# Performance work log

Measured on AMD Instinct MI355X. Metric: run time of the kernel, lower is better.

## Reference

```python
import jax, jax.numpy as jnp
import numpy as np

N = 4096       # rows (batch * points)
D = 512        # d_model
H = 8          # num_heads


def setup_inputs() -> dict:
    key = jax.random.key(0)
    ks = jax.random.split(key, 11)
    s = 1.0 / np.sqrt(D).astype(np.float32)
    return {
        "x_q": jax.random.normal(ks[0], (N, D), jnp.float32),
        "x_k": jax.random.normal(ks[1], (N, D), jnp.float32),
        "x_v": jax.random.normal(ks[2], (N, D), jnp.float32),
        "Wq": jax.random.normal(ks[3], (D, D), jnp.float32) * s,
        "bq": jax.random.normal(ks[4], (D,), jnp.float32) * s,
        "Wk": jax.random.normal(ks[5], (D, D), jnp.float32) * s,
        "bk": jax.random.normal(ks[6], (D,), jnp.float32) * s,
        "Wv": jax.random.normal(ks[7], (D, D), jnp.float32) * s,
        "bv": jax.random.normal(ks[8], (D,), jnp.float32) * s,
        "Wo": jax.random.normal(ks[9], (D, D), jnp.float32) * s,
        "bo": jax.random.normal(ks[10], (D,), jnp.float32) * s,
    }


def reference(x_q, x_k, x_v, Wq, bq, Wk, bk, Wv, bv, Wo, bo):
    n, d = x_q.shape
    d_k = d // H
    # linear projections
    q = (x_q @ Wq + bq).reshape(n, H, d_k)  # chunk(dim=-1) == head split
    k = (x_k @ Wk + bk).reshape(n, H, d_k)
    v = (x_v @ Wv + bv).reshape(n, H, d_k)
    # channel-wise outer-product attention: scores[n,h,i,j] = q_i * k_j / sqrt(d_k)
    scale = jnp.asarray(1.0 / np.sqrt(d_k), q.dtype)
    scores = q[..., :, None] * k[..., None, :] * scale  # (n, H, d_k, d_k)
    p = jax.nn.softmax(scores, axis=-1)
    # attn output: p @ v over channel axis -> (n, H, d_k)
    x = jnp.einsum('nhij,nhj->nhi', p, v).reshape(n, d)  # head merge (cat dim=-1)
    return (x_q - x) @ Wo + bo
```

## Files before the change

kernel.cpp:

```cpp
#include <hip/hip_runtime.h>
#include <hip/hip_bf16.h>

#define NROWS 4096
#define DMODEL 512
#define NHEAD 8
#define DKH 64
#define ND (NROWS * DMODEL)
#define DD (DMODEL * DMODEL)

typedef unsigned short u16;
typedef __attribute__((ext_vector_type(8))) short short8;
typedef __attribute__((ext_vector_type(4))) float floatx4;

__device__ __forceinline__ u16 f2b(float f) {
    unsigned u = __float_as_uint(f);
    unsigned r = (u + 0x7fffu + ((u >> 16) & 1u)) >> 16;
    return (u16)r;
}
__device__ __forceinline__ float b2f(u16 v) {
    return __uint_as_float(((unsigned)v) << 16);
}
__device__ __forceinline__ void async16(const void* g, void* l) {
    __builtin_amdgcn_global_load_lds(g, l, 16, 0, 0);
}

__global__ __launch_bounds__(256) void convert_x(
    const float* __restrict__ s0, const float* __restrict__ s1,
    const float* __restrict__ s2, u16* __restrict__ d0, u16* __restrict__ d1,
    u16* __restrict__ d2, int nElem) {
    const float* s = blockIdx.z == 0 ? s0 : (blockIdx.z == 1 ? s1 : s2);
    u16* d = blockIdx.z == 0 ? d0 : (blockIdx.z == 1 ? d1 : d2);
    int i = (blockIdx.x * blockDim.x + threadIdx.x) * 4;
    if (i < nElem) {
        float4 v = *(const float4*)(s + i);
        ushort4 o;
        o.x = f2b(v.x); o.y = f2b(v.y); o.z = f2b(v.z); o.w = f2b(v.w);
        *(ushort4*)(d + i) = o;
    }
}

__global__ __launch_bounds__(256) void convert_w(
    const float* __restrict__ W0, const float* __restrict__ W1,
    const float* __restrict__ W2, const float* __restrict__ W3,
    u16* __restrict__ T0, u16* __restrict__ T1, u16* __restrict__ T2,
    u16* __restrict__ T3) {
    __shared__ float tile[32][33];
    int z = blockIdx.z;
    const float* W = z == 0 ? W0 : (z == 1 ? W1 : (z == 2 ? W2 : W3));
    u16* T = z == 0 ? T0 : (z == 1 ? T1 : (z == 2 ? T2 : T3));
    int n0 = blockIdx.x * 32, k0 = blockIdx.y * 32;
    int tx = threadIdx.x, ty = threadIdx.y;
#pragma unroll
    for (int r = 0; r < 32; r += 8)
        tile[ty + r][tx] = W[(size_t)(k0 + ty + r) * DMODEL + n0 + tx];
    __syncthreads();
#pragma unroll
    for (int r = 0; r < 32; r += 8) {
        int n = n0 + ty + r, k = k0 + tx;
        T[(size_t)n * DMODEL + k] = f2b(tile[tx][ty + r]);
    }
}

template <int OUTF>
__device__ __forceinline__ void gemm_bt_body(const u16* __restrict__ A,
                                             const u16* __restrict__ Bt,
                                             const float* __restrict__ bias,
                                             void* __restrict__ Cout) {
    __shared__ __align__(16) u16 lA[128 * 32];
    __shared__ __align__(16) u16 lB[64 * 32];
    const int tid = threadIdx.x;
    const int wave = tid >> 6, lane = tid & 63;
    const int tileM = blockIdx.y * 128;
    const int tileN = blockIdx.x * 64;
    const int wm = wave >> 1, wn = wave & 1;

    floatx4 acc[4][2];
#pragma unroll
    for (int i = 0; i < 4; i++)
#pragma unroll
        for (int j = 0; j < 2; j++) acc[i][j] = (floatx4){0.f, 0.f, 0.f, 0.f};

    const int lr4 = lane >> 2;
    const int ls = lane & 3;
    const int lrow = lane & 15;
    const int sk = lane >> 4;

    for (int t = 0; t < 16; ++t) {
        const int k0 = t * 32;
#pragma unroll
        for (int i = 0; i < 2; i++) {
            int c = wave * 2 + i;
            int r = c * 16 + lr4;
            int s = ls ^ ((r >> 1) & 3);
            async16(A + (size_t)(tileM + r) * 512 + k0 + s * 8, &lA[c * 512]);
        }
        {
            int r = wave * 16 + lr4;
            int s = ls ^ ((r >> 1) & 3);
            async16(Bt + (size_t)(tileN + r) * 512 + k0 + s * 8, &lB[wave * 512]);
        }
        __syncthreads();

        short8 bfr[2];
#pragma unroll
        for (int ni = 0; ni < 2; ++ni) {
            int r = wn * 32 + ni * 16 + lrow;
            int s = sk ^ ((r >> 1) & 3);
            bfr[ni] = *(const short8*)&lB[r * 32 + s * 8];
        }
#pragma unroll
        for (int mi = 0; mi < 4; ++mi) {
            int r = wm * 64 + mi * 16 + lrow;
            int s = sk ^ ((r >> 1) & 3);
            short8 af = *(const short8*)&lA[r * 32 + s * 8];
#pragma unroll
            for (int ni = 0; ni < 2; ++ni)
                acc[mi][ni] = __builtin_amdgcn_mfma_f32_16x16x32_bf16(
                    af, bfr[ni], acc[mi][ni], 0, 0, 0);
        }
        __syncthreads();
    }

#pragma unroll
    for (int mi = 0; mi < 4; ++mi) {
#pragma unroll
        for (int ni = 0; ni < 2; ++ni) {
            int col = tileN + wn * 32 + ni * 16 + lrow;
            float bv = bias[col];
#pragma unroll
            for (int r2 = 0; r2 < 4; r2++) {
                int row = tileM + wm * 64 + mi * 16 + sk * 4 + r2;
                float val = acc[mi][ni][r2] + bv;
                if (OUTF)
                    ((float*)Cout)[(size_t)row * 512 + col] = val;
                else
                    ((u16*)Cout)[(size_t)row * 512 + col] = f2b(val);
            }
        }
    }
}

__global__ __launch_bounds__(256) void proj3(
    const u16* __restrict__ xq, const u16* __restrict__ xk,
    const u16* __restrict__ xv, const u16* __restrict__ wtq,
    const u16* __restrict__ wtk, const u16* __restrict__ wtv,
    const float* __restrict__ bq, const float* __restrict__ bk,
    const float* __restrict__ bv, u16* __restrict__ Q, u16* __restrict__ K,
    u16* __restrict__ V) {
    int z = blockIdx.z;
    const u16* A = z == 0 ? xq : (z == 1 ? xk : xv);
    const u16* Bt = z == 0 ? wtq : (z == 1 ? wtk : wtv);
    const float* bias = z == 0 ? bq : (z == 1 ? bk : bv);
    u16* C = z == 0 ? Q : (z == 1 ? K : V);
    gemm_bt_body<0>(A, Bt, bias, C);
}

__global__ __launch_bounds__(256) void out_gemm(const u16* __restrict__ T,
                                                const u16* __restrict__ wto,
                                                const float* __restrict__ bo,
                                                float* __restrict__ C) {
    gemm_bt_body<1>(T, wto, bo, C);
}

__global__ __launch_bounds__(256) void attn_kernel(
    const u16* __restrict__ Qb, const u16* __restrict__ Kb,
    const u16* __restrict__ Vb, const float* __restrict__ xq,
    u16* __restrict__ Tout) {
    __shared__ float lk[4][64];
    __shared__ float lv[4][64];
    const int wave = threadIdx.x >> 6, lane = threadIdx.x & 63;
    const int p = blockIdx.x * 4 + wave;
    const int n = p >> 3, h = p & 7;
    const size_t base = (size_t)n * DMODEL + h * DKH;

    float q = b2f(Qb[base + lane]);
    lk[wave][lane] = b2f(Kb[base + lane]) * 0.125f;
    lv[wave][lane] = b2f(Vb[base + lane]);
    __syncthreads();

    float num = 0.f, den = 0.f;
#pragma unroll
    for (int j = 0; j < 64; j += 4) {
        float4 kv = *(const float4*)&lk[wave][j];
        float4 vv = *(const float4*)&lv[wave][j];
        float e0 = __expf(q * kv.x);
        float e1 = __expf(q * kv.y);
        float e2 = __expf(q * kv.z);
        float e3 = __expf(q * kv.w);
        den += e0 + e1 + e2 + e3;
        num += e0 * vv.x + e1 * vv.y + e2 * vv.z + e3 * vv.w;
    }
    float t = xq[base + lane] - num / den;
    Tout[base + lane] = f2b(t);
}

extern "C" void kernel_launch(void* const* d_in, const int* in_sizes, int n_in,
                              void* d_out, int out_size, void* d_ws,
                              size_t ws_size, hipStream_t stream) {
    const float* x_q = (const float*)d_in[0];
    const float* x_k = (const float*)d_in[1];
    const float* x_v = (const float*)d_in[2];
    const float* Wq = (const float*)d_in[3];
    const float* bq = (const float*)d_in[4];
    const float* Wk = (const float*)d_in[5];
    const float* bk = (const float*)d_in[6];
    const float* Wv = (const float*)d_in[7];
    const float* bv = (const float*)d_in[8];
    const float* Wo = (const float*)d_in[9];
    const float* bo = (const float*)d_in[10];

    u16* ws = (u16*)d_ws;
    u16* xqb = ws;
    u16* xkb = xqb + ND;
    u16* xvb = xkb + ND;
    u16* wtq = xvb + ND;
    u16* wtk = wtq + DD;
    u16* wtv = wtk + DD;
    u16* wto = wtv + DD;
    u16* Qb = wto + DD;
    u16* Kb = Qb + ND;
    u16* Vb = Kb + ND;
    u16* Tb = Vb + ND;

    convert_x<<<dim3(ND / 4 / 256, 1, 3), 256, 0, stream>>>(x_q, x_k, x_v, xqb,
                                                            xkb, xvb, ND);
    convert_w<<<dim3(16, 16, 4), dim3(32, 8), 0, stream>>>(Wq, Wk, Wv, Wo, wtq,
                                                           wtk, wtv, wto);
    proj3<<<dim3(DMODEL / 64, NROWS / 128, 3), 256, 0, stream>>>(
        xqb, xkb, xvb, wtq, wtk, wtv, bq, bk, bv, Qb, Kb, Vb);
    attn_kernel<<<dim3(NROWS * NHEAD / 4), 256, 0, stream>>>(Qb, Kb, Vb, x_q,
                                                             Tb);
    out_gemm<<<dim3(DMODEL / 64, NROWS / 128), 256, 0, stream>>>(
        Tb, wto, bo, (float*)d_out);
}
```

Measured before the change: 145.2 us.

## Fuse x conversion, QKV projections and attention into one double-buffered kernel

Removes the separate fp32-to-bf16 conversion of activations and the standalone attention kernel. A single kernel now computes 64x64 tiles of Q, K and V for the same rows and head, converting fp32 x on the fly. It keeps the results in shared memory and applies the per-head channel softmax there before writing only T. Both GEMMs gain register/LDS double buffering, 64x64 tiles with a swizzled block order, and a two-blocks-per-CU launch bound. This cuts global traffic and launches, at the cost of larger shared memory use and serial attention work per wave inside the GEMM kernel.

```diff
diff --git a/kernel.cpp b/kernel.cpp
--- a/kernel.cpp
+++ b/kernel.cpp
@@ -23,20 +23,11 @@
 __device__ __forceinline__ void async16(const void* g, void* l) {
     __builtin_amdgcn_global_load_lds(g, l, 16, 0, 0);
 }
-
-__global__ __launch_bounds__(256) void convert_x(
-    const float* __restrict__ s0, const float* __restrict__ s1,
-    const float* __restrict__ s2, u16* __restrict__ d0, u16* __restrict__ d1,
-    u16* __restrict__ d2, int nElem) {
-    const float* s = blockIdx.z == 0 ? s0 : (blockIdx.z == 1 ? s1 : s2);
-    u16* d = blockIdx.z == 0 ? d0 : (blockIdx.z == 1 ? d1 : d2);
-    int i = (blockIdx.x * blockDim.x + threadIdx.x) * 4;
-    if (i < nElem) {
-        float4 v = *(const float4*)(s + i);
-        ushort4 o;
-        o.x = f2b(v.x); o.y = f2b(v.y); o.z = f2b(v.z); o.w = f2b(v.w);
-        *(ushort4*)(d + i) = o;
-    }
+__device__ __forceinline__ short8 cvt8(float4 a0, float4 a1) {
+    short8 av;
+    av[0] = f2b(a0.x); av[1] = f2b(a0.y); av[2] = f2b(a0.z); av[3] = f2b(a0.w);
+    av[4] = f2b(a1.x); av[5] = f2b(a1.y); av[6] = f2b(a1.z); av[7] = f2b(a1.w);
+    return av;
 }
 
 __global__ __launch_bounds__(256) void convert_w(
@@ -61,137 +52,219 @@
     }
 }
 
-template <int OUTF>
-__device__ __forceinline__ void gemm_bt_body(const u16* __restrict__ A,
-                                             const u16* __restrict__ Bt,
-                                             const float* __restrict__ bias,
-                                             void* __restrict__ Cout) {
-    __shared__ __align__(16) u16 lA[128 * 32];
-    __shared__ __align__(16) u16 lB[64 * 32];
+__global__ __launch_bounds__(256, 2) void proj_attn(
+    const float* __restrict__ xq, const float* __restrict__ xk,
+    const float* __restrict__ xv, const u16* __restrict__ wtq,
+    const u16* __restrict__ wtk, const u16* __restrict__ wtv,
+    const float* __restrict__ bq, const float* __restrict__ bk,
+    const float* __restrict__ bv, u16* __restrict__ Tb) {
+    __shared__ __align__(16) u16 smem[24576];
+
+    const int d = blockIdx.x;
+    const int id = (d & 7) * 64 + (d >> 3);
+    const int tileM = (id >> 3) * 64;
+    const int tileN = (id & 7) * 64;
+
+    const float* XA[3] = {xq, xk, xv};
+    const u16* WT[3] = {wtq, wtk, wtv};
+    const float* BIAS[3] = {bq, bk, bv};
+
     const int tid = threadIdx.x;
     const int wave = tid >> 6, lane = tid & 63;
-    const int tileM = blockIdx.y * 128;
-    const int tileN = blockIdx.x * 64;
     const int wm = wave >> 1, wn = wave & 1;
-
-    floatx4 acc[4][2];
-#pragma unroll
-    for (int i = 0; i < 4; i++)
+    const int lr4 = lane >> 2, ls = lane & 3;
+    const int lrow = lane & 15, sk = lane >> 4;
+
+    const int arow = tid >> 2, aslot = tid & 3;
+    const int asw = aslot ^ ((arow >> 1) & 3);
+    const float* aptr[3];
+#pragma unroll
+    for (int m = 0; m < 3; m++)
+        aptr[m] = XA[m] + (size_t)(tileM + arow) * 512 + aslot * 8;
+
+    floatx4 acc[3][2][2];
+#pragma unroll
+    for (int m = 0; m < 3; m++)
+#pragma unroll
+        for (int i = 0; i < 2; i++)
+#pragma unroll
+            for (int j = 0; j < 2; j++)
+                acc[m][i][j] = (floatx4){0.f, 0.f, 0.f, 0.f};
+
+#pragma unroll
+    for (int i = 0; i < 3; i++) {
+        int c = wave * 3 + i, m = c >> 2, ch = c & 3;
+        int r = ch * 16 + lr4, s = ls ^ ((r >> 1) & 3);
+        async16(WT[m] + (size_t)(tileN + r) * 512 + s * 8,
+                &smem[12288 + m * 2048 + ch * 512]);
+    }
+#pragma unroll
+    for (int m = 0; m < 3; m++) {
+        float4 a0 = *(const float4*)aptr[m];
+        float4 a1 = *(const float4*)(aptr[m] + 4);
+        *(short8*)&smem[m * 2048 + arow * 32 + asw * 8] = cvt8(a0, a1);
+    }
+    __syncthreads();
+
+    for (int t = 0; t < 16; ++t) {
+        const int cur = t & 1, nxt = cur ^ 1;
+        float4 na[3][2];
+        if (t < 15) {
+#pragma unroll
+            for (int m = 0; m < 3; m++) {
+                const float* p = aptr[m] + (t + 1) * 32;
+                na[m][0] = *(const float4*)p;
+                na[m][1] = *(const float4*)(p + 4);
+            }
+#pragma unroll
+            for (int i = 0; i < 3; i++) {
+                int c = wave * 3 + i, m = c >> 2, ch = c & 3;
+                int r = ch * 16 + lr4, s = ls ^ ((r >> 1) & 3);
+                async16(WT[m] + (size_t)(tileN + r) * 512 + (t + 1) * 32 + s * 8,
+                        &smem[12288 + (nxt * 3 + m) * 2048 + ch * 512]);
+            }
+        }
+#pragma unroll
+        for (int m = 0; m < 3; m++) {
+            short8 afr[2], bfr[2];
+#pragma unroll
+            for (int mi = 0; mi < 2; ++mi) {
+                int r = wm * 32 + mi * 16 + lrow;
+                int s = sk ^ ((r >> 1) & 3);
+                afr[mi] = *(const short8*)&smem[(cur * 3 + m) * 2048 + r * 32 + s * 8];
+            }
+#pragma unroll
+            for (int ni = 0; ni < 2; ++ni) {
+                int r = wn * 32 + ni * 16 + lrow;
+                int s = sk ^ ((r >> 1) & 3);
+                bfr[ni] = *(const short8*)&smem[12288 + (cur * 3 + m) * 2048 + r * 32 + s * 8];
+            }
+#pragma unroll
+            for (int mi = 0; mi < 2; ++mi)
+#pragma unroll
+                for (int ni = 0; ni < 2; ++ni)
+                    acc[m][mi][ni] = __builtin_amdgcn_mfma_f32_16x16x32_bf16(
+                        afr[mi], bfr[ni], acc[m][mi][ni], 0, 0, 0);
+        }
+        if (t < 15) {
+#pragma unroll
+            for (int m = 0; m < 3; m++)
+                *(short8*)&smem[(nxt * 3 + m) * 2048 + arow * 32 + asw * 8] =
+                    cvt8(na[m][0], na[m][1]);
+        }
+        __syncthreads();
+    }
+
+#pragma unroll
+    for (int m = 0; m < 3; m++) {
+#pragma unroll
+        for (int mi = 0; mi < 2; ++mi)
+#pragma unroll
+            for (int ni = 0; ni < 2; ++ni) {
+                int col = wn * 32 + ni * 16 + lrow;
+                float bv_ = BIAS[m][tileN + col];
+#pragma unroll
+                for (int r2 = 0; r2 < 4; r2++) {
+                    int row = wm * 32 + mi * 16 + sk * 4 + r2;
+                    smem[m * 4352 + row * 68 + col] =
+                        f2b(acc[m][mi][ni][r2] + bv_);
+                }
+            }
+    }
+    __syncthreads();
+
+    const u16* lq = smem;
+    const u16* lk = smem + 4352;
+    const u16* lv = smem + 8704;
+    for (int i = 0; i < 16; ++i) {
+        int nl = wave * 16 + i;
+        float qs = b2f(lq[nl * 68 + lane]) * 0.125f;
+        float num = 0.f, den = 0.f;
+#pragma unroll
+        for (int j = 0; j < 64; ++j) {
+            float kj = b2f(lk[nl * 68 + j]);
+            float vj = b2f(lv[nl * 68 + j]);
+            float e = __expf(qs * kj);
+            den += e;
+            num += e * vj;
+        }
+        size_t gi = (size_t)(tileM + nl) * 512 + tileN + lane;
+        Tb[gi] = f2b(xq[gi] - num / den);
+    }
+}
+
+__global__ __launch_bounds__(256, 2) void out_gemm(const u16* __restrict__ T,
+                                                   const u16* __restrict__ wto,
+                                                   const float* __restrict__ bo,
+                                                   float* __restrict__ C) {
+    __shared__ __align__(16) u16 sA[2][2048];
+    __shared__ __align__(16) u16 sB[2][2048];
+    const int d = blockIdx.x;
+    const int id = (d & 7) * 64 + (d >> 3);
+    const int tileM = (id >> 3) * 64;
+    const int tileN = (id & 7) * 64;
+
+    const int tid = threadIdx.x;
+    const int wave = tid >> 6, lane = tid & 63;
+    const int wm = wave >> 1, wn = wave & 1;
+    const int lr4 = lane >> 2, ls = lane & 3;
+    const int lrow = lane & 15, sk = lane >> 4;
+
+    const int r0 = wave * 16 + lr4;
+    const int s0 = ls ^ ((r0 >> 1) & 3);
+    const u16* aptr = T + (size_t)(tileM + r0) * 512 + s0 * 8;
+    const u16* bptr = wto + (size_t)(tileN + r0) * 512 + s0 * 8;
+
+    floatx4 acc[2][2];
+#pragma unroll
+    for (int i = 0; i < 2; i++)
 #pragma unroll
         for (int j = 0; j < 2; j++) acc[i][j] = (floatx4){0.f, 0.f, 0.f, 0.f};
 
-    const int lr4 = lane >> 2;
-    const int ls = lane & 3;
-    const int lrow = lane & 15;
-    const int sk = lane >> 4;
+    async16(aptr, &sA[0][wave * 512]);
+    async16(bptr, &sB[0][wave * 512]);
+    __syncthreads();
 
     for (int t = 0; t < 16; ++t) {
-        const int k0 = t * 32;
-#pragma unroll
-        for (int i = 0; i < 2; i++) {
-            int c = wave * 2 + i;
-            int r = c * 16 + lr4;
-            int s = ls ^ ((r >> 1) & 3);
-            async16(A + (size_t)(tileM + r) * 512 + k0 + s * 8, &lA[c * 512]);
-        }
-        {
-            int r = wave * 16 + lr4;
-            int s = ls ^ ((r >> 1) & 3);
-            async16(Bt + (size_t)(tileN + r) * 512 + k0 + s * 8, &lB[wave * 512]);
-        }
-        __syncthreads();
-
-        short8 bfr[2];
+        const int cur = t & 1, nxt = cur ^ 1;
+        if (t < 15) {
+            async16(aptr + (t + 1) * 32, &sA[nxt][wave * 512]);
+            async16(bptr + (t + 1) * 32, &sB[nxt][wave * 512]);
+        }
+        short8 afr[2], bfr[2];
+#pragma unroll
+        for (int mi = 0; mi < 2; ++mi) {
+            int r = wm * 32 + mi * 16 + lrow;
+            int s = sk ^ ((r >> 1) & 3);
+            afr[mi] = *(const short8*)&sA[cur][r * 32 + s * 8];
+        }
 #pragma unroll
         for (int ni = 0; ni < 2; ++ni) {
             int r = wn * 32 + ni * 16 + lrow;
             int s = sk ^ ((r >> 1) & 3);
-            bfr[ni] = *(const short8*)&lB[r * 32 + s * 8];
-        }
-#pragma unroll
-        for (int mi = 0; mi < 4; ++mi) {
-            int r = wm * 64 + mi * 16 + lrow;
-            int s = sk ^ ((r >> 1) & 3);
-            short8 af = *(const short8*)&lA[r * 32 + s * 8];
+            bfr[ni] = *(const short8*)&sB[cur][r * 32 + s * 8];
+        }
+#pragma unroll
+        for (int mi = 0; mi < 2; ++mi)
 #pragma unroll
             for (int ni = 0; ni < 2; ++ni)
                 acc[mi][ni] = __builtin_amdgcn_mfma_f32_16x16x32_bf16(
-                    af, bfr[ni], acc[mi][ni], 0, 0, 0);
-        }
+                    afr[mi], bfr[ni], acc[mi][ni], 0, 0, 0);
         __syncthreads();
     }
 
 #pragma unroll
-    for (int mi = 0; mi < 4; ++mi) {
+    for (int mi = 0; mi < 2; ++mi)
 #pragma unroll
         for (int ni = 0; ni < 2; ++ni) {
             int col = tileN + wn * 32 + ni * 16 + lrow;
-            float bv = bias[col];
+            float bv = bo[col];
 #pragma unroll
             for (int r2 = 0; r2 < 4; r2++) {
-                int row = tileM + wm * 64 + mi * 16 + sk * 4 + r2;
-                float val = acc[mi][ni][r2] + bv;
-                if (OUTF)
-                    ((float*)Cout)[(size_t)row * 512 + col] = val;
-                else
-                    ((u16*)Cout)[(size_t)row * 512 + col] = f2b(val);
-            }
-        }
-    }
-}
-
-__global__ __launch_bounds__(256) void proj3(
-    const u16* __restrict__ xq, const u16* __restrict__ xk,
-    const u16* __restrict__ xv, const u16* __restrict__ wtq,
-    const u16* __restrict__ wtk, const u16* __restrict__ wtv,
-    const float* __restrict__ bq, const float* __restrict__ bk,
-    const float* __restrict__ bv, u16* __restrict__ Q, u16* __restrict__ K,
-    u16* __restrict__ V) {
-    int z = blockIdx.z;
-    const u16* A = z == 0 ? xq : (z == 1 ? xk : xv);
-    const u16* Bt = z == 0 ? wtq : (z == 1 ? wtk : wtv);
-    const float* bias = z == 0 ? bq : (z == 1 ? bk : bv);
-    u16* C = z == 0 ? Q : (z == 1 ? K : V);
-    gemm_bt_body<0>(A, Bt, bias, C);
-}
-
-__global__ __launch_bounds__(256) void out_gemm(const u16* __restrict__ T,
-                                                const u16* __restrict__ wto,
-                                                const float* __restrict__ bo,
-                                                float* __restrict__ C) {
-    gemm_bt_body<1>(T, wto, bo, C);
-}
-
-__global__ __launch_bounds__(256) void attn_kernel(
-    const u16* __restrict__ Qb, const u16* __restrict__ Kb,
-    const u16* __restrict__ Vb, const float* __restrict__ xq,
-    u16* __restrict__ Tout) {
-    __shared__ float lk[4][64];
-    __shared__ float lv[4][64];
-    const int wave = threadIdx.x >> 6, lane = threadIdx.x & 63;
-    const int p = blockIdx.x * 4 + wave;
-    const int n = p >> 3, h = p & 7;
-    const size_t base = (size_t)n * DMODEL + h * DKH;
-
-    float q = b2f(Qb[base + lane]);
-    lk[wave][lane] = b2f(Kb[base + lane]) * 0.125f;
-    lv[wave][lane] = b2f(Vb[base + lane]);
-    __syncthreads();
-
-    float num = 0.f, den = 0.f;
-#pragma unroll
-    for (int j = 0; j < 64; j += 4) {
-        float4 kv = *(const float4*)&lk[wave][j];
-        float4 vv = *(const float4*)&lv[wave][j];
-        float e0 = __expf(q * kv.x);
-        float e1 = __expf(q * kv.y);
-        float e2 = __expf(q * kv.z);
-        float e3 = __expf(q * kv.w);
-        den += e0 + e1 + e2 + e3;
-        num += e0 * vv.x + e1 * vv.y + e2 * vv.z + e3 * vv.w;
-    }
-    float t = xq[base + lane] - num / den;
-    Tout[base + lane] = f2b(t);
+                int row = tileM + wm * 32 + mi * 16 + sk * 4 + r2;
+                C[(size_t)row * 512 + col] = acc[mi][ni][r2] + bv;
+            }
+        }
 }
 
 extern "C" void kernel_launch(void* const* d_in, const int* in_sizes, int n_in,
@@ -210,26 +283,15 @@
     const float* bo = (const float*)d_in[10];
 
     u16* ws = (u16*)d_ws;
-    u16* xqb = ws;
-    u16* xkb = xqb + ND;
-    u16* xvb = xkb + ND;
-    u16* wtq = xvb + ND;
+    u16* wtq = ws;
     u16* wtk = wtq + DD;
     u16* wtv = wtk + DD;
     u16* wto = wtv + DD;
-    u16* Qb = wto + DD;
-    u16* Kb = Qb + ND;
-    u16* Vb = Kb + ND;
-    u16* Tb = Vb + ND;
-
-    convert_x<<<dim3(ND / 4 / 256, 1, 3), 256, 0, stream>>>(x_q, x_k, x_v, xqb,
-                                                            xkb, xvb, ND);
+    u16* Tb = wto + DD;
+
     convert_w<<<dim3(16, 16, 4), dim3(32, 8), 0, stream>>>(Wq, Wk, Wv, Wo, wtq,
                                                            wtk, wtv, wto);
-    proj3<<<dim3(DMODEL / 64, NROWS / 128, 3), 256, 0, stream>>>(
-        xqb, xkb, xvb, wtq, wtk, wtv, bq, bk, bv, Qb, Kb, Vb);
-    attn_kernel<<<dim3(NROWS * NHEAD / 4), 256, 0, stream>>>(Qb, Kb, Vb, x_q,
-                                                             Tb);
-    out_gemm<<<dim3(DMODEL / 64, NROWS / 128), 256, 0, stream>>>(
-        Tb, wto, bo, (float*)d_out);
-}
+    proj_attn<<<dim3(512), 256, 0, stream>>>(x_q, x_k, x_v, wtq, wtk, wtv, bq,
+                                             bk, bv, Tb);
+    out_gemm<<<dim3(512), 256, 0, stream>>>(Tb, wto, bo, (float*)d_out);
+}
```

Measured after the change: 153.0 us. +5.4%, slower.
